# Kernel tuning notes

Measured on AMD Instinct MI355X. Metric: run time of the kernel, lower is better.

Reference implementation:

```python
import jax, jax.numpy as jnp
import numpy as np

B_SZ, SEQ, D_MODEL, D_STATE, KSIZE = 8, 4096, 1024, 64, 64
DT_MIN, DT_MAX = 0.001, 0.1


def setup_inputs() -> dict:
    key = jax.random.key(0)
    k1, k2, k3, k4 = jax.random.split(key, 4)
    u = jax.random.normal(k1, (B_SZ, SEQ, D_MODEL), dtype=jnp.float32)
    # HiPPO-like init: A = -(n+1)
    A = -(jnp.arange(D_STATE, dtype=jnp.float32) + 1.0)
    Bp = 0.01 * jax.random.normal(k2, (D_STATE, D_MODEL), dtype=jnp.float32)
    Cp = 0.01 * jax.random.normal(k3, (D_MODEL, D_STATE), dtype=jnp.float32)
    Dp = jnp.ones((D_MODEL,), dtype=jnp.float32)
    log_dt = jnp.log(jax.random.uniform(k4, (D_MODEL,), dtype=jnp.float32,
                                        minval=DT_MIN, maxval=DT_MAX))
    return {"u": u, "A": A, "B": Bp, "C": Cp, "D": Dp, "log_dt": log_dt}


def reference(u, A, B, C, D, log_dt):
    # u: (batch, seq_len, d_model)
    batch, seq_len, d_model = u.shape
    L = min(seq_len, KSIZE)  # truncated SSM kernel length

    # --- SSM kernel (same math as ssm_kernel) ---
    dt = jnp.exp(log_dt)                         # (d_model,)
    A_bar = jnp.exp(A[:, None] * dt[None, :])    # (d_state, d_model)
    powers = jnp.arange(L)[:, None, None]        # (L,1,1)
    A_powers = A_bar[None, :, :] ** powers       # (L, d_state, d_model)
    # K[l,k] = sum_{m,d} C[m,d] * A_bar[d,k]^l * B[d,k]  (faithful to original einsum)
    K = jnp.einsum('md,ldk,dk->lk', C, A_powers, B)  # (L, d_model)

    # --- Batched per-channel 'same' convolution via FFT ---
    # Equivalent to jnp.convolve(u[b,:,i], K[:,i], mode='same') for every b, i,
    # with L <= seq_len so the 'same' slice starts at (L-1)//2.
    n = seq_len + L - 1
    Uf = jnp.fft.rfft(u, n=n, axis=1)            # (batch, nf, d_model)
    Kf = jnp.fft.rfft(K, n=n, axis=0)            # (nf, d_model)
    conv_full = jnp.fft.irfft(Uf * Kf[None], n=n, axis=1)  # (batch, n, d_model)
    start = (L - 1) // 2
    y = conv_full[:, start:start + seq_len, :]

    # skip connection
    y = y + D[None, None, :] * u
    return y
```

## Files before the change

### kernel.cpp

```cpp
#include <hip/hip_runtime.h>

#define SEQ 4096
#define DM 1024
#define DS 64
#define KS 64
#define R 16

__global__ void csum_kernel(const float* __restrict__ C, float* __restrict__ csum) {
    int d    = threadIdx.x & 63;
    int mloc = threadIdx.x >> 6;
    int m0   = blockIdx.x * 64;
    float s = 0.f;
#pragma unroll
    for (int j = 0; j < 16; ++j) {
        int m = m0 + j * 4 + mloc;
        s += C[m * DS + d];
    }
    __shared__ float red[4][64];
    red[mloc][d] = s;
    __syncthreads();
    if (threadIdx.x < 64) {
        float t = red[0][d] + red[1][d] + red[2][d] + red[3][d];
        atomicAdd(&csum[d], t);
    }
}

__global__ void taps_kernel(const float* __restrict__ A, const float* __restrict__ B,
                            const float* __restrict__ log_dt,
                            const float* __restrict__ csum, float* __restrict__ Kt) {
    int g = blockIdx.x * blockDim.x + threadIdx.x;
    int l = g & 63;
    int k = g >> 6;
    float dt = __expf(log_dt[k]);
    float fl = (float)l;
    float acc = 0.f;
#pragma unroll 8
    for (int d = 0; d < DS; ++d) {
        acc += csum[d] * __expf(A[d] * dt * fl) * B[d * DM + k];
    }
    Kt[k * KS + l] = acc;
}

__global__ __launch_bounds__(256)
void conv_kernel(const float* __restrict__ u, const float* __restrict__ Kt,
                 const float* __restrict__ D, float* __restrict__ y) {
    __shared__ float taps[64 * 65];

    int k0 = blockIdx.x * 64;
    int t0 = blockIdx.y * 64;
    int b  = blockIdx.z;

    for (int i = threadIdx.x; i < 64 * 64; i += 256) {
        int kk = i >> 6, l = i & 63;
        taps[kk * 65 + l] = Kt[(k0 + kk) * KS + l];
    }
    __syncthreads();

    int kl = threadIdx.x & 63;
    int wv = threadIdx.x >> 6;
    int ts = t0 + wv * R;

    const float* up = u + (size_t)b * SEQ * DM + k0 + kl;

    float w[R + 63];
    int tw0 = ts - 32;
#pragma unroll
    for (int i = 0; i < R + 63; ++i) {
        int t = tw0 + i;
        w[i] = (t >= 0 && t < SEQ) ? up[(size_t)t * DM] : 0.f;
    }

    float acc[R];
#pragma unroll
    for (int r = 0; r < R; ++r) acc[r] = 0.f;

#pragma unroll
    for (int l = 0; l < 64; ++l) {
        float tap = taps[kl * 65 + l];
#pragma unroll
        for (int r = 0; r < R; ++r)
            acc[r] = fmaf(tap, w[r + 63 - l], acc[r]);
    }

    float Dk = D[k0 + kl];
    float* yp = y + ((size_t)b * SEQ + ts) * DM + k0 + kl;
#pragma unroll
    for (int r = 0; r < R; ++r)
        yp[(size_t)r * DM] = fmaf(Dk, w[r + 32], acc[r]);
}

extern "C" void kernel_launch(void* const* d_in, const int* in_sizes, int n_in,
                              void* d_out, int out_size, void* d_ws, size_t ws_size,
                              hipStream_t stream) {
    const float* u      = (const float*)d_in[0];
    const float* A      = (const float*)d_in[1];
    const float* Bp     = (const float*)d_in[2];
    const float* Cp     = (const float*)d_in[3];
    const float* Dp     = (const float*)d_in[4];
    const float* log_dt = (const float*)d_in[5];
    float* y = (float*)d_out;

    float* csum = (float*)d_ws;
    float* Kt   = csum + 64;

    hipMemsetAsync(csum, 0, DS * sizeof(float), stream);
    csum_kernel<<<16, 256, 0, stream>>>(Cp, csum);
    taps_kernel<<<(DM * KS) / 256, 256, 0, stream>>>(A, Bp, log_dt, csum, Kt);

    dim3 grid(DM / 64, SEQ / 64, 8);
    conv_kernel<<<grid, 256, 0, stream>>>(u, Kt, Dp, y);
}
```

Baseline: 274.8 us.

## Restructure conv with float2 channel pairs, sliding register window, interior fast path

Each thread now handles two adjacent channels through float2 loads and stores, and the time tile doubles to 128 per block. The input window is kept in a 31-entry register ring that is refilled in four chunks of 16, instead of preloading 79 values. Taps are stored transposed in shared memory and read as float2. A guard-free template path serves interior tiles. The aim is wider memory transactions, lower register pressure and no bounds checks in the inner loop, in exchange for more complex indexing and a two-path kernel.

```diff
diff --git a/kernel.cpp b/kernel.cpp
--- a/kernel.cpp
+++ b/kernel.cpp
@@ -4,7 +4,10 @@
 #define DM 1024
 #define DS 64
 #define KS 64
-#define R 16
+
+#define TCH 64
+#define TT  128
+#define R   16
 
 __global__ void csum_kernel(const float* __restrict__ C, float* __restrict__ csum) {
     int d    = threadIdx.x & 63;
@@ -12,10 +15,8 @@
     int m0   = blockIdx.x * 64;
     float s = 0.f;
 #pragma unroll
-    for (int j = 0; j < 16; ++j) {
-        int m = m0 + j * 4 + mloc;
-        s += C[m * DS + d];
-    }
+    for (int j = 0; j < 16; ++j)
+        s += C[(m0 + j * 4 + mloc) * DS + d];
     __shared__ float red[4][64];
     red[mloc][d] = s;
     __syncthreads();
@@ -27,66 +28,100 @@
 
 __global__ void taps_kernel(const float* __restrict__ A, const float* __restrict__ B,
                             const float* __restrict__ log_dt,
-                            const float* __restrict__ csum, float* __restrict__ Kt) {
+                            const float* __restrict__ csum, float* __restrict__ Ktl) {
     int g = blockIdx.x * blockDim.x + threadIdx.x;
-    int l = g & 63;
-    int k = g >> 6;
+    int k = g & (DM - 1);
+    int l = g >> 10;
     float dt = __expf(log_dt[k]);
     float fl = (float)l;
     float acc = 0.f;
 #pragma unroll 8
-    for (int d = 0; d < DS; ++d) {
+    for (int d = 0; d < DS; ++d)
         acc += csum[d] * __expf(A[d] * dt * fl) * B[d * DM + k];
+    Ktl[g] = acc;
+}
+
+template<bool GUARD>
+__device__ __forceinline__ float2 ldu(const float2* __restrict__ up2, int t) {
+    if (GUARD) {
+        if (t >= 0 && t < SEQ) return up2[(size_t)t * (DM / 2)];
+        return make_float2(0.f, 0.f);
     }
-    Kt[k * KS + l] = acc;
+    return up2[(size_t)t * (DM / 2)];
+}
+
+template<bool GUARD>
+__device__ __forceinline__ void do_tile(const float2* __restrict__ up2,
+                                        float2* __restrict__ yp2,
+                                        const float (*tapsL)[66],
+                                        float2 D2, int ts, int c2) {
+    float2 acc[R];
+#pragma unroll
+    for (int r = 0; r < R; ++r) acc[r] = make_float2(0.f, 0.f);
+
+    float2 w[31];
+#pragma unroll
+    for (int i = 0; i < 31; ++i) w[i] = ldu<GUARD>(up2, ts + 16 + i);
+
+#pragma unroll
+    for (int c = 0; c < 4; ++c) {
+        if (c > 0) {
+#pragma unroll
+            for (int i = 30; i >= 16; --i) w[i] = w[i - 16];
+            int wb = ts + 16 - 16 * c;
+#pragma unroll
+            for (int i = 0; i < 16; ++i) w[i] = ldu<GUARD>(up2, wb + i);
+        }
+        if (c == 1) {
+#pragma unroll
+            for (int r = 0; r < R; ++r) {
+                acc[r].x = fmaf(D2.x, w[r].x, acc[r].x);
+                acc[r].y = fmaf(D2.y, w[r].y, acc[r].y);
+            }
+        }
+#pragma unroll
+        for (int j = 0; j < 16; ++j) {
+            float2 t2 = *(const float2*)&tapsL[16 * c + j][2 * c2];
+#pragma unroll
+            for (int r = 0; r < R; ++r) {
+                acc[r].x = fmaf(t2.x, w[r + 15 - j].x, acc[r].x);
+                acc[r].y = fmaf(t2.y, w[r + 15 - j].y, acc[r].y);
+            }
+        }
+    }
+
+#pragma unroll
+    for (int r = 0; r < R; ++r)
+        yp2[(size_t)(ts + r) * (DM / 2)] = acc[r];
 }
 
 __global__ __launch_bounds__(256)
-void conv_kernel(const float* __restrict__ u, const float* __restrict__ Kt,
+void conv_kernel(const float* __restrict__ u, const float* __restrict__ Ktl,
                  const float* __restrict__ D, float* __restrict__ y) {
-    __shared__ float taps[64 * 65];
+    __shared__ __align__(16) float tapsL[KS][66];
 
-    int k0 = blockIdx.x * 64;
-    int t0 = blockIdx.y * 64;
+    int k0 = blockIdx.x * TCH;
+    int t0 = blockIdx.y * TT;
     int b  = blockIdx.z;
 
-    for (int i = threadIdx.x; i < 64 * 64; i += 256) {
-        int kk = i >> 6, l = i & 63;
-        taps[kk * 65 + l] = Kt[(k0 + kk) * KS + l];
+    for (int i = threadIdx.x; i < KS * TCH; i += 256) {
+        int l = i >> 6, kk = i & 63;
+        tapsL[l][kk] = Ktl[l * DM + k0 + kk];
     }
     __syncthreads();
 
-    int kl = threadIdx.x & 63;
-    int wv = threadIdx.x >> 6;
-    int ts = t0 + wv * R;
+    int c2 = threadIdx.x & 31;
+    int tg = threadIdx.x >> 5;
+    int ts = t0 + tg * R;
+    int p  = (k0 >> 1) + c2;
 
-    const float* up = u + (size_t)b * SEQ * DM + k0 + kl;
+    const float2* up2 = (const float2*)u + (size_t)b * SEQ * (DM / 2) + p;
+    float2*       yp2 = (float2*)y       + (size_t)b * SEQ * (DM / 2) + p;
+    float2 D2 = *(const float2*)(D + k0 + 2 * c2);
 
-    float w[R + 63];
-    int tw0 = ts - 32;
-#pragma unroll
-    for (int i = 0; i < R + 63; ++i) {
-        int t = tw0 + i;
-        w[i] = (t >= 0 && t < SEQ) ? up[(size_t)t * DM] : 0.f;
-    }
-
-    float acc[R];
-#pragma unroll
-    for (int r = 0; r < R; ++r) acc[r] = 0.f;
-
-#pragma unroll
-    for (int l = 0; l < 64; ++l) {
-        float tap = taps[kl * 65 + l];
-#pragma unroll
-        for (int r = 0; r < R; ++r)
-            acc[r] = fmaf(tap, w[r + 63 - l], acc[r]);
-    }
-
-    float Dk = D[k0 + kl];
-    float* yp = y + ((size_t)b * SEQ + ts) * DM + k0 + kl;
-#pragma unroll
-    for (int r = 0; r < R; ++r)
-        yp[(size_t)r * DM] = fmaf(Dk, w[r + 32], acc[r]);
+    bool interior = (t0 >= 32) && (t0 + 159 <= SEQ);
+    if (interior) do_tile<false>(up2, yp2, tapsL, D2, ts, c2);
+    else          do_tile<true >(up2, yp2, tapsL, D2, ts, c2);
 }
 
 extern "C" void kernel_launch(void* const* d_in, const int* in_sizes, int n_in,
@@ -101,12 +136,12 @@
     float* y = (float*)d_out;
 
     float* csum = (float*)d_ws;
-    float* Kt   = csum + 64;
+    float* Ktl  = csum + 64;
 
     hipMemsetAsync(csum, 0, DS * sizeof(float), stream);
     csum_kernel<<<16, 256, 0, stream>>>(Cp, csum);
-    taps_kernel<<<(DM * KS) / 256, 256, 0, stream>>>(A, Bp, log_dt, csum, Kt);
+    taps_kernel<<<(DM * KS) / 256, 256, 0, stream>>>(A, Bp, log_dt, csum, Ktl);
 
-    dim3 grid(DM / 64, SEQ / 64, 8);
-    conv_kernel<<<grid, 256, 0, stream>>>(u, Kt, Dp, y);
+    dim3 grid(DM / TCH, SEQ / TT, 8);
+    conv_kernel<<<grid, 256, 0, stream>>>(u, Ktl, Dp, y);
 }
```

New measurement: 312.6 us. 1.14x slower.
